# Performance work log

Hardware: AMD Instinct MI355X
Metric: run time of the kernel (lower is better)

## Reference

```python
import jax, jax.numpy as jnp
import numpy as np

N, E, G = 100000, 1600000, 8
IN, H, OUT = 3, 64, 20


def setup_inputs() -> dict:
    key = jax.random.key(0)
    ks = jax.random.split(key, 24)
    def nrm(k, shape, scale=0.1):
        return jax.random.normal(k, shape, dtype=jnp.float32) * scale
    inp = {}
    inp["x"] = jax.random.normal(ks[0], (N, IN), dtype=jnp.float32)
    inp["edge_index"] = jax.random.randint(ks[1], (2, E), 0, N, dtype=jnp.int32)
    inp["batch"] = jnp.sort(jax.random.randint(ks[2], (N,), 0, G, dtype=jnp.int32))
    dims = [(IN, H), (H, H), (H, H)]  # 3 GATConv layers (initial + layers-1)
    for i, (di, do) in enumerate(dims):
        inp[f"W{i}"] = nrm(ks[3 + 4 * i], (di, do))
        inp[f"as{i}"] = nrm(ks[4 + 4 * i], (do,))
        inp[f"ad{i}"] = nrm(ks[5 + 4 * i], (do,))
        inp[f"b{i}"] = jnp.zeros((do,), jnp.float32)
    inp["vn_emb0"] = jnp.zeros((1, H), jnp.float32)  # constant-0 init per module
    inp["m1_w1"] = nrm(ks[15], (H, H)); inp["m1_b1"] = jnp.zeros((H,), jnp.float32)
    inp["m1_w2"] = nrm(ks[16], (H, H)); inp["m1_b2"] = jnp.zeros((H,), jnp.float32)
    inp["mf_w1"] = nrm(ks[17], (H, H)); inp["mf_b1"] = jnp.zeros((H,), jnp.float32)
    inp["mf_w2"] = nrm(ks[18], (H, OUT)); inp["mf_b2"] = jnp.zeros((OUT,), jnp.float32)
    inp["out_w"] = nrm(ks[19], (H, OUT)); inp["out_b"] = jnp.zeros((OUT,), jnp.float32)
    return inp


def _gat(x, src, dst, W, a_s, a_d, b):
    # PyG GATConv, 1 head: h = xW; e_ij = LeakyReLU_0.2(a_s.h_j + a_d.h_i);
    # alpha = softmax over incoming edges of each dst node; out_i = sum_j alpha_ij h_j + b
    h = x @ W                                                  # [N, H]
    lg = jax.nn.leaky_relu((h @ a_s)[src] + (h @ a_d)[dst], 0.2)  # [E+N]
    m = jax.ops.segment_max(lg, dst, num_segments=N)
    m = jnp.where(jnp.isfinite(m), m, 0.0)
    p = jnp.exp(lg - m[dst])
    denom = jax.ops.segment_sum(p, dst, num_segments=N)
    alpha = p / denom[dst]
    return jax.ops.segment_sum(alpha[:, None] * h[src], dst, num_segments=N) + b


def _forward(x, edge_index, batch, params):
    (W0, as0, ad0, b0, W1, as1, ad1, b1, W2, as2, ad2, b2,
     vn_emb0, m1_w1, m1_b1, m1_w2, m1_b2, mf_w1, mf_b1, mf_w2, mf_b2,
     out_w, out_b) = params
    loops = jnp.arange(N, dtype=edge_index.dtype)  # GATConv add_self_loops=True
    src = jnp.concatenate([edge_index[0], loops])
    dst = jnp.concatenate([edge_index[1], loops])
    act = lambda v: jax.nn.leaky_relu(v, 0.01)  # nn.LeakyReLU default slope
    h = act(_gat(x, src, dst, W0, as0, ad0, b0))
    h = act(_gat(h, src, dst, W1, as1, ad1, b1))
    h = act(_gat(h, src, dst, W2, as2, ad2, b2))
    # virtual node: global_add_pool(out, batch) + Embedding(0) (zero-init)
    vn = jax.ops.segment_sum(h, batch, num_segments=G) + vn_emb0[0]
    vn = jax.nn.relu(vn @ m1_w1 + m1_b1)
    vn = jax.nn.relu(vn @ m1_w2 + m1_b2)
    vn = jax.nn.relu(vn @ mf_w1 + mf_b1)
    vn = jax.nn.relu(vn @ mf_w2 + mf_b2)
    return (h @ out_w + out_b, vn)


def reference(x, edge_index, batch, W0, as0, ad0, b0, W1, as1, ad1, b1,
              W2, as2, ad2, b2, vn_emb0, m1_w1, m1_b1, m1_w2, m1_b2,
              mf_w1, mf_b1, mf_w2, mf_b2, out_w, out_b):
    params = (W0, as0, ad0, b0, W1, as1, ad1, b1, W2, as2, ad2, b2,
              vn_emb0, m1_w1, m1_b1, m1_w2, m1_b2, mf_w1, mf_b1, mf_w2, mf_b2,
              out_w, out_b)
    return _forward(x, edge_index, batch, params)
```

## Files before the change

kernel.cpp:

```cpp
#include <hip/hip_runtime.h>
#include <hip/hip_bf16.h>

#define H 64
#define OUTD 20
#define NGRAPH 8
#define NBK 256
#define CAPB 8192
#define MAXDEG 63

typedef __attribute__((ext_vector_type(8))) short bf16x8;
typedef __attribute__((ext_vector_type(4))) float f32x4;
typedef __attribute__((ext_vector_type(8))) unsigned short u16x8;


__device__ __forceinline__ float ldp(const void* p, int i, bool f32) {
    return f32 ? ((const float*)p)[i]
               : __bfloat162float(((const __hip_bfloat16*)p)[i]);
}

__device__ __forceinline__ float bfu(unsigned short u) {
    union { unsigned int i; float f; } c; c.i = ((unsigned)u) << 16; return c.f;
}
__device__ __forceinline__ unsigned short fbits(float f) {
    __hip_bfloat16 b = __float2bfloat16(f);
    return *reinterpret_cast<unsigned short*>(&b);
}

__global__ void detect_dtype(const unsigned short* __restrict__ xb, int n_u16,
                             int* __restrict__ flag, int* __restrict__ gcur,
                             int* __restrict__ gtot, float* __restrict__ vnp,
                             float* __restrict__ s, short* __restrict__ hbuf,
                             int n, int ns) {
    __shared__ int sh[256];
    int t = threadIdx.x;
    int m = min(n_u16, 4096);
    int bad = 0;
    for (int i = t; i < m; i += 256) {
        unsigned e = (xb[i] >> 7) & 0xFF;
        bad += (e >= 0x90) ? 1 : 0;
    }
    sh[t] = bad;
    if (t < NBK) gcur[t] = 0;
    for (int i = t; i < NGRAPH * H; i += 256) vnp[i] = 0.f;
    if (t < 32) hbuf[(size_t)n * 32 + t] = 0;
    else if (t < 64) hbuf[((size_t)ns + n) * 32 + (t - 32)] = 0;
    if (t == 0) { *gtot = 0; s[n] = -1e30f; }
    __syncthreads();
    for (int off = 128; off; off >>= 1) {
        if (t < off) sh[t] += sh[t + off];
        __syncthreads();
    }
    if (t == 0) *flag = (sh[0] > (m >> 4)) ? 1 : 0;
}

__global__ void fillC_dense0(const int* __restrict__ src, const int* __restrict__ dst,
                             int* __restrict__ gcur, unsigned* __restrict__ ebuf,
                             int E, int n, int ns, int nC, int EPC, int nbk,
                             const void* __restrict__ x, const void* __restrict__ W,
                             const void* __restrict__ a_s, const void* __restrict__ a_d,
                             __hip_bfloat16* __restrict__ h, float* __restrict__ s,
                             float* __restrict__ d, const int* __restrict__ flagp) {
    if ((int)blockIdx.x < nC) {
        __shared__ unsigned lcnt[NBK];
        __shared__ int lbase[NBK];
        int t = threadIdx.x;
        for (int i = t; i < NBK; i += 256) lcnt[i] = 0;
        __syncthreads();
        int base = blockIdx.x * (256 * EPC) + t;
        int dnr[8];
        for (int i = 0; i < EPC; ++i) {
            int e = base + i * 256;
            int dn = (e < E) ? dst[e] : -1;
            if (i < 8) dnr[i] = dn;
            if ((unsigned)dn < (unsigned)n) atomicAdd(&lcnt[dn >> 9], 1u);
        }
        __syncthreads();
        for (int i = t; i < nbk; i += 256) {
            unsigned c = lcnt[i];
            lbase[i] = c ? atomicAdd(&gcur[i], (int)c) : 0;
            lcnt[i] = 0;
        }
        __syncthreads();
        for (int i = 0; i < EPC; ++i) {
            int e = base + i * 256;
            if (e < E) {
                int dn = (i < 8) ? dnr[i] : dst[e];
                if ((unsigned)dn < (unsigned)n) {
                    int b = dn >> 9;
                    unsigned pos = (unsigned)lbase[b] + atomicAdd(&lcnt[b], 1u);
                    if (pos < CAPB)
                        ebuf[(size_t)b * CAPB + pos] =
                            ((unsigned)src[e] << 9) | (unsigned)(dn & 511);
                }
            }
        }
        return;
    }
    const bool f32 = (*flagp != 0);
    int idx = ((int)blockIdx.x - nC) * 256 + threadIdx.x;
    int node = idx >> 6;
    int f = idx & 63;
    if (node >= n) return;
    float acc = 0.f;
    for (int k = 0; k < 3; ++k)
        acc += ldp(x, node * 3 + k, f32) * ldp(W, k * H + f, f32);
    ((short*)h)[((size_t)(f >> 5) * ns + node) * 32 + (f & 31)] = (short)fbits(acc);
    float sv = acc * ldp(a_s, f, f32);
    float dv = acc * ldp(a_d, f, f32);
    for (int off = 32; off; off >>= 1) {
        sv += __shfl_xor(sv, off);
        dv += __shfl_xor(dv, off);
    }
    if (f == 0) { s[node] = sv; d[node] = dv; }
}

__global__ __launch_bounds__(512) void bucketD(const unsigned* __restrict__ ebuf,
                                               const int* __restrict__ gcur,
                                               unsigned* __restrict__ cntoff,
                                               int* __restrict__ col,
                                               int* __restrict__ gtot, int n) {
    __shared__ unsigned lcnt[512];
    __shared__ int loff[512];
    __shared__ int sdeg[512];
    __shared__ int wpart[8];
    __shared__ int sbase, stot;
    int b = blockIdx.x, t = threadIdx.x;
    lcnt[t] = 0;
    __syncthreads();
    int end = min(gcur[b], CAPB);
    const unsigned* reg = ebuf + (size_t)b * CAPB;
    for (int i = t; i < end; i += 512) atomicAdd(&lcnt[reg[i] & 511u], 1u);
    __syncthreads();
    int node = (b << 9) + t;
    int degc = (node < n) ? (int)min(lcnt[t], (unsigned)MAXDEG) : 0;
    int Dp = (node < n) ? ((degc + 1 <= 24) ? 24 : 64) : 0;
    int lane = t & 63, wid = t >> 6;
    int xs = Dp;
    for (int o = 1; o < 64; o <<= 1) {
        int v = __shfl_up(xs, o);
        if (lane >= o) xs += v;
    }
    if (lane == 63) wpart[wid] = xs;
    __syncthreads();
    if (t == 0) {
        int acc = 0;
        for (int w8 = 0; w8 < 8; ++w8) { int v = wpart[w8]; wpart[w8] = acc; acc += v; }
        stot = acc;
        sbase = atomicAdd(gtot, acc);
    }
    __syncthreads();
    int myoff = sbase + wpart[wid] + xs - Dp;
    loff[t] = myoff;
    sdeg[t] = degc;
    if (node < n) cntoff[node] = (unsigned)myoff | ((unsigned)Dp << 24);
    lcnt[t] = 0;
    int total = stot;
    for (int i = t; i < total; i += 512) col[sbase + i] = n;
    __syncthreads();
    if (node < n) col[myoff + degc] = node;
    for (int i = t; i < end; i += 512) {
        unsigned e = reg[i];
        int loc = (int)(e & 511u);
        unsigned pos = atomicAdd(&lcnt[loc], 1u);
        if ((int)pos < sdeg[loc])
            col[loff[loc] + pos] = (int)(e >> 9);
    }
}

#define ACC8(w, hv) { \
    a[0] += w * bfu(hv[0]); a[1] += w * bfu(hv[1]); \
    a[2] += w * bfu(hv[2]); a[3] += w * bfu(hv[3]); \
    a[4] += w * bfu(hv[4]); a[5] += w * bfu(hv[5]); \
    a[6] += w * bfu(hv[6]); a[7] += w * bfu(hv[7]); }

__global__ void gat_agg_sliced(const short* __restrict__ hs,
                               const float* __restrict__ s,
                               const float* __restrict__ d,
                               const unsigned* __restrict__ cntoff,
                               const int* __restrict__ col,
                               const void* __restrict__ bias,
                               short* __restrict__ outs, int n, int ns,
                               const int* __restrict__ flagp) {
    const bool f32 = (*flagp != 0);
    int shp = (int)blockIdx.x & 7;
    int fh = shp >> 2, nq = shp & 3;
    int qN = (n + 3) >> 2;
    int node = nq * qN + ((int)blockIdx.x >> 3) * 8 + ((int)threadIdx.x >> 5);
    int lim = min(n, (nq + 1) * qN);
    if (node >= lim) return;
    int l = threadIdx.x & 31;
    int c = l & 3, q = l >> 2;
    unsigned co = cntoff[node];
    bool big = (int)(co >> 24) > 24;
    const int* cb = col + (co & 0xFFFFFFu);
    const char* hb = (const char*)hs + (size_t)fh * ns * 64;
    float di = d[node];
    unsigned coff = (unsigned)c * 16u;

    int s0 = cb[q];
    int s1 = cb[q + 8];
    int s2 = cb[q + 16];
    float v0 = s[s0] + di, v1 = s[s1] + di, v2 = s[s2] + di;
    u16x8 hv0 = *(const u16x8*)(hb + ((unsigned)s0 * 64u + coff));
    u16x8 hv1 = *(const u16x8*)(hb + ((unsigned)s1 * 64u + coff));
    u16x8 hv2 = *(const u16x8*)(hb + ((unsigned)s2 * 64u + coff));
    float sv0 = v0 > 0.f ? v0 : 0.2f * v0;
    float sv1 = v1 > 0.f ? v1 : 0.2f * v1;
    float sv2 = v2 > 0.f ? v2 : 0.2f * v2;

    float sv3 = -INFINITY, sv4 = -INFINITY, sv5 = -INFINITY,
          sv6 = -INFINITY, sv7 = -INFINITY;
    u16x8 hv3 = {}, hv4 = {}, hv5 = {}, hv6 = {}, hv7 = {};
    if (big) {
        int s3 = cb[q + 24];
        int s4 = cb[q + 32];
        int s5 = cb[q + 40];
        int s6 = cb[q + 48];
        int s7 = cb[q + 56];
        float v3 = s[s3] + di, v4 = s[s4] + di, v5 = s[s5] + di,
              v6 = s[s6] + di, v7 = s[s7] + di;
        hv3 = *(const u16x8*)(hb + ((unsigned)s3 * 64u + coff));
        hv4 = *(const u16x8*)(hb + ((unsigned)s4 * 64u + coff));
        hv5 = *(const u16x8*)(hb + ((unsigned)s5 * 64u + coff));
        hv6 = *(const u16x8*)(hb + ((unsigned)s6 * 64u + coff));
        hv7 = *(const u16x8*)(hb + ((unsigned)s7 * 64u + coff));
        sv3 = v3 > 0.f ? v3 : 0.2f * v3;
        sv4 = v4 > 0.f ? v4 : 0.2f * v4;
        sv5 = v5 > 0.f ? v5 : 0.2f * v5;
        sv6 = v6 > 0.f ? v6 : 0.2f * v6;
        sv7 = v7 > 0.f ? v7 : 0.2f * v7;
    }

    float mx = fmaxf(fmaxf(fmaxf(sv0, sv1), fmaxf(sv2, sv3)),
                     fmaxf(fmaxf(sv4, sv5), fmaxf(sv6, sv7)));
    mx = fmaxf(mx, __shfl_xor(mx, 4));
    mx = fmaxf(mx, __shfl_xor(mx, 8));
    mx = fmaxf(mx, __shfl_xor(mx, 16));

    float w0 = __expf(sv0 - mx);
    float w1 = __expf(sv1 - mx);
    float w2 = __expf(sv2 - mx);
    float wsum = w0 + w1 + w2;

    float a[8] = {0.f, 0.f, 0.f, 0.f, 0.f, 0.f, 0.f, 0.f};
    ACC8(w0, hv0);
    ACC8(w1, hv1);
    ACC8(w2, hv2);
    if (big) {
        float w3 = __expf(sv3 - mx);
        float w4 = __expf(sv4 - mx);
        float w5 = __expf(sv5 - mx);
        float w6 = __expf(sv6 - mx);
        float w7 = __expf(sv7 - mx);
        wsum += w3 + w4 + w5 + w6 + w7;
        ACC8(w3, hv3);
        ACC8(w4, hv4);
        ACC8(w5, hv5);
        ACC8(w6, hv6);
        ACC8(w7, hv7);
    }
    wsum += __shfl_xor(wsum, 4);
    wsum += __shfl_xor(wsum, 8);
    wsum += __shfl_xor(wsum, 16);
#pragma unroll
    for (int i = 0; i < 8; ++i) {
        a[i] += __shfl_xor(a[i], 4);
        a[i] += __shfl_xor(a[i], 8);
        a[i] += __shfl_xor(a[i], 16);
    }
    if (q == 0) {
        float inv = 1.f / fmaxf(wsum, 1e-20f);
        u16x8 ov;
        for (int i = 0; i < 8; ++i) {
            float o = a[i] * inv + ldp(bias, fh * 32 + c * 8 + i, f32);
            o = o > 0.f ? o : 0.01f * o;
            ov[i] = fbits(o);
        }
        ((u16x8*)outs)[((size_t)fh * ns + node) * 4 + c] = ov;
    }
}


__global__ __launch_bounds__(256) void denseN_mfma(
    const __hip_bfloat16* __restrict__ in,
    const void* __restrict__ W,
    const void* __restrict__ a_s, const void* __restrict__ a_d,
    __hip_bfloat16* __restrict__ h, float* __restrict__ s,
    float* __restrict__ d, int n, int ns, const int* __restrict__ flagp) {
    const bool f32 = (*flagp != 0);
    __shared__ short Wt[64 * 72];
    int t = threadIdx.x;
    for (int i = t; i < 4096; i += 256) {
        int k = i >> 6, nf = i & 63;
        Wt[nf * 72 + k] = (short)fbits(ldp(W, i, f32));
    }
    __syncthreads();

    int wid = t >> 6, lane = t & 63;
    int quad = lane >> 4, n16 = lane & 15;
    int nodeBase = blockIdx.x * 64 + wid * 16;
    int mrow = nodeBase + n16;
    int mclamp = min(mrow, n - 1);
    const short* inp = (const short*)in;
    bf16x8 a0 = *(const bf16x8*)(inp + (size_t)mclamp * 32 + quad * 8);
    bf16x8 a1 = *(const bf16x8*)(inp + ((size_t)ns + mclamp) * 32 + quad * 8);

    float as_v[4], ad_v[4];
    for (int nt = 0; nt < 4; ++nt) {
        as_v[nt] = ldp(a_s, nt * 16 + n16, f32);
        ad_v[nt] = ldp(a_d, nt * 16 + n16, f32);
    }

    float sv[4] = {0.f, 0.f, 0.f, 0.f}, dv[4] = {0.f, 0.f, 0.f, 0.f};
    f32x4 accs[4];
    for (int nt = 0; nt < 4; ++nt) {
        const short* wrow = Wt + (nt * 16 + n16) * 72;
        bf16x8 b0 = *(const bf16x8*)(wrow + quad * 8);
        bf16x8 b1 = *(const bf16x8*)(wrow + 32 + quad * 8);
        f32x4 cacc = {0.f, 0.f, 0.f, 0.f};
        cacc = __builtin_amdgcn_mfma_f32_16x16x32_bf16(a0, b0, cacc, 0, 0, 0);
        cacc = __builtin_amdgcn_mfma_f32_16x16x32_bf16(a1, b1, cacc, 0, 0, 0);
        accs[nt] = cacc;
        for (int r = 0; r < 4; ++r) {
            sv[r] += cacc[r] * as_v[nt];
            dv[r] += cacc[r] * ad_v[nt];
        }
    }

    short* hb = (short*)h;
    for (int r = 0; r < 4; ++r) {
        int node = nodeBase + quad * 4 + r;
        if (node < n) {
            for (int nt = 0; nt < 4; ++nt) {
                int f = nt * 16 + n16;
                hb[((size_t)(f >> 5) * ns + node) * 32 + (f & 31)] = (short)fbits(accs[nt][r]);
            }
        }
    }
    for (int r = 0; r < 4; ++r) {
        for (int mask = 1; mask < 16; mask <<= 1) {
            sv[r] += __shfl_xor(sv[r], mask);
            dv[r] += __shfl_xor(dv[r], mask);
        }
    }
    if (n16 == 0) {
        for (int r = 0; r < 4; ++r) {
            int node = nodeBase + quad * 4 + r;
            if (node < n) { s[node] = sv[r]; d[node] = dv[r]; }
        }
    }
}


__global__ __launch_bounds__(256) void proj_pool(
    const __hip_bfloat16* __restrict__ h,
    const void* __restrict__ W, const void* __restrict__ b,
    void* __restrict__ out, int n, int ns, const int* __restrict__ flagp,
    int projBlocks, const int* __restrict__ batch, float* __restrict__ vn) {
    const bool f32 = (*flagp != 0);
    if ((int)blockIdx.x < projBlocks) {
        __shared__ short Wt[32 * 72];
        int t = threadIdx.x;
        for (int i = t; i < 32 * 64; i += 256) {
            int o = i >> 6, k = i & 63;
            Wt[o * 72 + k] = (o < OUTD) ? (short)fbits(ldp(W, k * OUTD + o, f32)) : 0;
        }
        __syncthreads();

        int wid = t >> 6, lane = t & 63;
        int quad = lane >> 4, n16 = lane & 15;
        int nodeBase = blockIdx.x * 64 + wid * 16;
        int mclamp = min(nodeBase + n16, n - 1);
        const short* hsrc = (const short*)h;
        bf16x8 a0 = *(const bf16x8*)(hsrc + (size_t)mclamp * 32 + quad * 8);
        bf16x8 a1 = *(const bf16x8*)(hsrc + ((size_t)ns + mclamp) * 32 + quad * 8);

        f32x4 acc0 = {0.f, 0.f, 0.f, 0.f}, acc1 = {0.f, 0.f, 0.f, 0.f};
        {
            const short* wrow = Wt + n16 * 72;
            bf16x8 b0 = *(const bf16x8*)(wrow + quad * 8);
            bf16x8 b1 = *(const bf16x8*)(wrow + 32 + quad * 8);
            acc0 = __builtin_amdgcn_mfma_f32_16x16x32_bf16(a0, b0, acc0, 0, 0, 0);
            acc0 = __builtin_amdgcn_mfma_f32_16x16x32_bf16(a1, b1, acc0, 0, 0, 0);
        }
        {
            const short* wrow = Wt + (16 + n16) * 72;
            bf16x8 b0 = *(const bf16x8*)(wrow + quad * 8);
            bf16x8 b1 = *(const bf16x8*)(wrow + 32 + quad * 8);
            acc1 = __builtin_amdgcn_mfma_f32_16x16x32_bf16(a0, b0, acc1, 0, 0, 0);
            acc1 = __builtin_amdgcn_mfma_f32_16x16x32_bf16(a1, b1, acc1, 0, 0, 0);
        }
        float bv0 = ldp(b, n16, f32);
        float bv1 = (n16 < OUTD - 16) ? ldp(b, 16 + n16, f32) : 0.f;
        for (int r = 0; r < 4; ++r) {
            int node = nodeBase + quad * 4 + r;
            if (node >= n) break;
            float o0 = acc0[r] + bv0;
            if (f32) ((float*)out)[node * OUTD + n16] = o0;
            else     ((__hip_bfloat16*)out)[node * OUTD + n16] = __float2bfloat16(o0);
            if (n16 < OUTD - 16) {
                float o1 = acc1[r] + bv1;
                if (f32) ((float*)out)[node * OUTD + 16 + n16] = o1;
                else     ((__hip_bfloat16*)out)[node * OUTD + 16 + n16] = __float2bfloat16(o1);
            }
        }
        return;
    }
    __shared__ float part[NGRAPH * H];
    int t = threadIdx.x;
    for (int i = t; i < NGRAPH * H; i += 256) part[i] = 0.f;
    __syncthreads();
    int pb = (int)blockIdx.x - projBlocks;
    int npb = gridDim.x - projBlocks;
    int wid = t >> 6, lane = t & 63;
    int gwave = pb * 4 + wid;
    int nwaves = npb * 4;
    int chunk = (n + nwaves - 1) / nwaves;
    int beg = gwave * chunk;
    int end = min(n, beg + chunk);
    if (beg < end) {
        const short* hb = (const short*)h + (size_t)(lane >> 5) * ns * 32 + (lane & 31);
        float acc = 0.f;
        int cur = batch[beg];
        for (int i = beg; i < end; ++i) {
            int g = batch[i];
            if (g != cur) {
                if ((unsigned)cur < NGRAPH) atomicAdd(&part[cur * H + lane], acc);
                acc = 0.f;
                cur = g;
            }
            acc += bfu((unsigned short)hb[(size_t)i * 32]);
        }
        if ((unsigned)cur < NGRAPH) atomicAdd(&part[cur * H + lane], acc);
    }
    __syncthreads();
    for (int i = t; i < NGRAPH * H; i += 256) {
        float v = part[i];
        if (v != 0.f) atomicAdd(&vn[i], v);
    }
}


__global__ void vn_mlp(const float* __restrict__ vn, const void* __restrict__ emb,
                       const void* __restrict__ w1, const void* __restrict__ b1,
                       const void* __restrict__ w2, const void* __restrict__ b2,
                       const void* __restrict__ w3, const void* __restrict__ b3,
                       const void* __restrict__ w4, const void* __restrict__ b4,
                       void* __restrict__ out, int out1_off, const int* __restrict__ flagp) {
    const bool f32 = (*flagp != 0);
    __shared__ float A[NGRAPH * H], B[NGRAPH * H];
    int t = threadIdx.x;
    int g = t >> 6, f = t & 63;
    A[t] = vn[t] + ldp(emb, f, f32);
    __syncthreads();
    float acc = ldp(b1, f, f32);
    for (int k = 0; k < H; ++k) acc += A[g * H + k] * ldp(w1, k * H + f, f32);
    B[t] = fmaxf(acc, 0.f);
    __syncthreads();
    acc = ldp(b2, f, f32);
    for (int k = 0; k < H; ++k) acc += B[g * H + k] * ldp(w2, k * H + f, f32);
    A[t] = fmaxf(acc, 0.f);
    __syncthreads();
    acc = ldp(b3, f, f32);
    for (int k = 0; k < H; ++k) acc += A[g * H + k] * ldp(w3, k * H + f, f32);
    B[t] = fmaxf(acc, 0.f);
    __syncthreads();
    if (f < OUTD) {
        acc = ldp(b4, f, f32);
        for (int k = 0; k < H; ++k) acc += B[g * H + k] * ldp(w4, k * OUTD + f, f32);
        acc = fmaxf(acc, 0.f);
        int idx = out1_off + g * OUTD + f;
        if (f32) ((float*)out)[idx] = acc;
        else     ((__hip_bfloat16*)out)[idx] = __float2bfloat16(acc);
    }
}


extern "C" void kernel_launch(void* const* d_in, const int* in_sizes, int n_in,
                              void* d_out, int out_size, void* d_ws, size_t ws_size,
                              hipStream_t stream) {
    const void* x   = d_in[0];
    const int* ei   = (const int*)d_in[1];
    const int* batch= (const int*)d_in[2];
    const void* W0  = d_in[3];
    const void* as0 = d_in[4];
    const void* ad0 = d_in[5];
    const void* b0  = d_in[6];
    const void* W1  = d_in[7];
    const void* as1 = d_in[8];
    const void* ad1 = d_in[9];
    const void* b1  = d_in[10];
    const void* W2  = d_in[11];
    const void* as2 = d_in[12];
    const void* ad2 = d_in[13];
    const void* b2  = d_in[14];
    const void* vne = d_in[15];
    const void* m1w1 = d_in[16];
    const void* m1b1 = d_in[17];
    const void* m1w2 = d_in[18];
    const void* m1b2 = d_in[19];
    const void* mfw1 = d_in[20];
    const void* mfb1 = d_in[21];
    const void* mfw2 = d_in[22];
    const void* mfb2 = d_in[23];
    const void* outw = d_in[24];
    const void* outb = d_in[25];

    const int N = in_sizes[2];
    const int E = in_sizes[1] / 2;
    const int NS = N + 1;
    const int* srcp = ei;
    const int* dstp = ei + E;

    char* w = (char*)d_ws;
    auto alloc = [&](size_t bytes) -> void* {
        void* p = (void*)w;
        w += ((bytes + 255) / 256) * 256;
        return p;
    };
    int*   flag   = (int*)alloc(256);
    int*   gcur   = (int*)alloc((size_t)NBK * 4);
    int*   gtot   = (int*)alloc(256);
    unsigned* ebuf= (unsigned*)alloc((size_t)NBK * CAPB * 4);
    unsigned* cntoff = (unsigned*)alloc((size_t)N * 4);
    int*   col    = (int*)alloc(((size_t)N * 64 + 64) * 4);
    __hip_bfloat16* featA = (__hip_bfloat16*)alloc((size_t)NS * H * 2);
    __hip_bfloat16* featB = (__hip_bfloat16*)alloc((size_t)NS * H * 2);
    __hip_bfloat16* hbuf  = (__hip_bfloat16*)alloc((size_t)NS * H * 2);
    float* sArr   = (float*)alloc((size_t)NS * 4);
    float* dArr   = (float*)alloc((size_t)N * 4);
    float* vn     = (float*)alloc((size_t)NGRAPH * H * 4);

    const int nbN64 = (N * H + 255) / 256;
    const int nb64 = (N + 63) / 64;
    const int projBlocks = (N + 63) / 64;
    const int nbk = (N + 511) >> 9;
    const int qN = (N + 3) >> 2;
    const int aggBlocks = 8 * ((qN + 7) / 8);
    int EPC = 8;
    int nC = (E + 256 * EPC - 1) / (256 * EPC);
    while (nC > 1024) { EPC <<= 1; nC = (E + 256 * EPC - 1) / (256 * EPC); }

    detect_dtype<<<1, 256, 0, stream>>>((const unsigned short*)x, in_sizes[0], flag,
                                        gcur, gtot, vn, sArr, (short*)hbuf, N, NS);

    fillC_dense0<<<nC + nbN64, 256, 0, stream>>>(
        srcp, dstp, gcur, ebuf, E, N, NS, nC, EPC, nbk,
        x, W0, as0, ad0, hbuf, sArr, dArr, flag);
    bucketD<<<nbk, 512, 0, stream>>>(ebuf, gcur, cntoff, col, gtot, N);

    gat_agg_sliced<<<aggBlocks, 256, 0, stream>>>((const short*)hbuf, sArr, dArr,
                                                  cntoff, col, b0, (short*)featA, N, NS, flag);
    denseN_mfma<<<nb64, 256, 0, stream>>>(featA, W1, as1, ad1, hbuf, sArr, dArr, N, NS, flag);
    gat_agg_sliced<<<aggBlocks, 256, 0, stream>>>((const short*)hbuf, sArr, dArr,
                                                  cntoff, col, b1, (short*)featB, N, NS, flag);
    denseN_mfma<<<nb64, 256, 0, stream>>>(featB, W2, as2, ad2, hbuf, sArr, dArr, N, NS, flag);
    gat_agg_sliced<<<aggBlocks, 256, 0, stream>>>((const short*)hbuf, sArr, dArr,
                                                  cntoff, col, b2, (short*)featA, N, NS, flag);

    proj_pool<<<projBlocks + 512, 256, 0, stream>>>(featA, outw, outb, d_out, N, NS, flag,
                                                    projBlocks, batch, vn);
    vn_mlp<<<1, 512, 0, stream>>>(vn, vne, m1w1, m1b1, m1w2, m1b2, mfw1, mfb1, mfw2, mfb2,
                                  d_out, N * OUTD, flag);
}
```

Measured before the change: 427.2 us.

## Split features into four 16-wide slices and aggregate with two lanes per node

Changes the bf16 feature layout from two 32-feature slices to four 16-feature slices (32 bytes per node row) across all producer and consumer kernels. The aggregation kernel now assigns two lanes per node per quarter slice, each lane walking the node's neighbour list serially. Degree-24 nodes take an unrolled path; other nodes use an online-softmax loop over blocks of 8. This drops the cross-lane shuffle reductions and makes each gather smaller, but adds serial per-lane work and more total index and score loads, since every slice re-reads the neighbour list.

```diff
diff --git a/kernel.cpp b/kernel.cpp
--- a/kernel.cpp
+++ b/kernel.cpp
@@ -42,8 +42,8 @@
     sh[t] = bad;
     if (t < NBK) gcur[t] = 0;
     for (int i = t; i < NGRAPH * H; i += 256) vnp[i] = 0.f;
-    if (t < 32) hbuf[(size_t)n * 32 + t] = 0;
-    else if (t < 64) hbuf[((size_t)ns + n) * 32 + (t - 32)] = 0;
+    if (t < 64)
+        hbuf[(size_t)(t >> 4) * ns * 16 + (size_t)n * 16 + (t & 15)] = 0;
     if (t == 0) { *gtot = 0; s[n] = -1e30f; }
     __syncthreads();
     for (int off = 128; off; off >>= 1) {
@@ -104,7 +104,8 @@
     float acc = 0.f;
     for (int k = 0; k < 3; ++k)
         acc += ldp(x, node * 3 + k, f32) * ldp(W, k * H + f, f32);
-    ((short*)h)[((size_t)(f >> 5) * ns + node) * 32 + (f & 31)] = (short)fbits(acc);
+    ((short*)h)[(size_t)(f >> 4) * ns * 16 + (size_t)node * 16 + (f & 15)] =
+        (short)fbits(acc);
     float sv = acc * ldp(a_s, f, f32);
     float dv = acc * ldp(a_d, f, f32);
     for (int off = 32; off; off >>= 1) {
@@ -167,117 +168,122 @@
     }
 }
 
-#define ACC8(w, hv) { \
-    a[0] += w * bfu(hv[0]); a[1] += w * bfu(hv[1]); \
-    a[2] += w * bfu(hv[2]); a[3] += w * bfu(hv[3]); \
-    a[4] += w * bfu(hv[4]); a[5] += w * bfu(hv[5]); \
-    a[6] += w * bfu(hv[6]); a[7] += w * bfu(hv[7]); }
-
-__global__ void gat_agg_sliced(const short* __restrict__ hs,
-                               const float* __restrict__ s,
-                               const float* __restrict__ d,
-                               const unsigned* __restrict__ cntoff,
-                               const int* __restrict__ col,
-                               const void* __restrict__ bias,
-                               short* __restrict__ outs, int n, int ns,
-                               const int* __restrict__ flagp) {
+__global__ void gat_agg_q(const short* __restrict__ hs,
+                          const float* __restrict__ s,
+                          const float* __restrict__ d,
+                          const unsigned* __restrict__ cntoff,
+                          const int* __restrict__ col,
+                          const void* __restrict__ bias,
+                          short* __restrict__ outs, int n, int ns, int halfN,
+                          const int* __restrict__ flagp) {
     const bool f32 = (*flagp != 0);
     int shp = (int)blockIdx.x & 7;
-    int fh = shp >> 2, nq = shp & 3;
-    int qN = (n + 3) >> 2;
-    int node = nq * qN + ((int)blockIdx.x >> 3) * 8 + ((int)threadIdx.x >> 5);
-    int lim = min(n, (nq + 1) * qN);
+    int fq = shp >> 1, nh = shp & 1;
+    int node = nh * halfN + ((int)blockIdx.x >> 3) * 128 + ((int)threadIdx.x >> 1);
+    int lim = nh ? n : halfN;
     if (node >= lim) return;
-    int l = threadIdx.x & 31;
-    int c = l & 3, q = l >> 2;
+    int c = threadIdx.x & 1;
     unsigned co = cntoff[node];
-    bool big = (int)(co >> 24) > 24;
     const int* cb = col + (co & 0xFFFFFFu);
-    const char* hb = (const char*)hs + (size_t)fh * ns * 64;
+    const char* hq = (const char*)hs + (size_t)fq * ns * 32 + c * 16;
     float di = d[node];
-    unsigned coff = (unsigned)c * 16u;
-
-    int s0 = cb[q];
-    int s1 = cb[q + 8];
-    int s2 = cb[q + 16];
-    float v0 = s[s0] + di, v1 = s[s1] + di, v2 = s[s2] + di;
-    u16x8 hv0 = *(const u16x8*)(hb + ((unsigned)s0 * 64u + coff));
-    u16x8 hv1 = *(const u16x8*)(hb + ((unsigned)s1 * 64u + coff));
-    u16x8 hv2 = *(const u16x8*)(hb + ((unsigned)s2 * 64u + coff));
-    float sv0 = v0 > 0.f ? v0 : 0.2f * v0;
-    float sv1 = v1 > 0.f ? v1 : 0.2f * v1;
-    float sv2 = v2 > 0.f ? v2 : 0.2f * v2;
-
-    float sv3 = -INFINITY, sv4 = -INFINITY, sv5 = -INFINITY,
-          sv6 = -INFINITY, sv7 = -INFINITY;
-    u16x8 hv3 = {}, hv4 = {}, hv5 = {}, hv6 = {}, hv7 = {};
-    if (big) {
-        int s3 = cb[q + 24];
-        int s4 = cb[q + 32];
-        int s5 = cb[q + 40];
-        int s6 = cb[q + 48];
-        int s7 = cb[q + 56];
-        float v3 = s[s3] + di, v4 = s[s4] + di, v5 = s[s5] + di,
-              v6 = s[s6] + di, v7 = s[s7] + di;
-        hv3 = *(const u16x8*)(hb + ((unsigned)s3 * 64u + coff));
-        hv4 = *(const u16x8*)(hb + ((unsigned)s4 * 64u + coff));
-        hv5 = *(const u16x8*)(hb + ((unsigned)s5 * 64u + coff));
-        hv6 = *(const u16x8*)(hb + ((unsigned)s6 * 64u + coff));
-        hv7 = *(const u16x8*)(hb + ((unsigned)s7 * 64u + coff));
-        sv3 = v3 > 0.f ? v3 : 0.2f * v3;
-        sv4 = v4 > 0.f ? v4 : 0.2f * v4;
-        sv5 = v5 > 0.f ? v5 : 0.2f * v5;
-        sv6 = v6 > 0.f ? v6 : 0.2f * v6;
-        sv7 = v7 > 0.f ? v7 : 0.2f * v7;
-    }
-
-    float mx = fmaxf(fmaxf(fmaxf(sv0, sv1), fmaxf(sv2, sv3)),
-                     fmaxf(fmaxf(sv4, sv5), fmaxf(sv6, sv7)));
-    mx = fmaxf(mx, __shfl_xor(mx, 4));
-    mx = fmaxf(mx, __shfl_xor(mx, 8));
-    mx = fmaxf(mx, __shfl_xor(mx, 16));
-
-    float w0 = __expf(sv0 - mx);
-    float w1 = __expf(sv1 - mx);
-    float w2 = __expf(sv2 - mx);
-    float wsum = w0 + w1 + w2;
-
-    float a[8] = {0.f, 0.f, 0.f, 0.f, 0.f, 0.f, 0.f, 0.f};
-    ACC8(w0, hv0);
-    ACC8(w1, hv1);
-    ACC8(w2, hv2);
-    if (big) {
-        float w3 = __expf(sv3 - mx);
-        float w4 = __expf(sv4 - mx);
-        float w5 = __expf(sv5 - mx);
-        float w6 = __expf(sv6 - mx);
-        float w7 = __expf(sv7 - mx);
-        wsum += w3 + w4 + w5 + w6 + w7;
-        ACC8(w3, hv3);
-        ACC8(w4, hv4);
-        ACC8(w5, hv5);
-        ACC8(w6, hv6);
-        ACC8(w7, hv7);
-    }
-    wsum += __shfl_xor(wsum, 4);
-    wsum += __shfl_xor(wsum, 8);
-    wsum += __shfl_xor(wsum, 16);
-#pragma unroll
-    for (int i = 0; i < 8; ++i) {
-        a[i] += __shfl_xor(a[i], 4);
-        a[i] += __shfl_xor(a[i], 8);
-        a[i] += __shfl_xor(a[i], 16);
-    }
-    if (q == 0) {
-        float inv = 1.f / fmaxf(wsum, 1e-20f);
-        u16x8 ov;
-        for (int i = 0; i < 8; ++i) {
-            float o = a[i] * inv + ldp(bias, fh * 32 + c * 8 + i, f32);
-            o = o > 0.f ? o : 0.01f * o;
-            ov[i] = fbits(o);
-        }
-        ((u16x8*)outs)[((size_t)fh * ns + node) * 4 + c] = ov;
-    }
+
+    float acc0 = 0.f, acc1 = 0.f, acc2 = 0.f, acc3 = 0.f,
+          acc4 = 0.f, acc5 = 0.f, acc6 = 0.f, acc7 = 0.f;
+    float wsum = 0.f;
+
+#define FMA8(w, hv) { \
+    acc0 += w * bfu(hv[0]); acc1 += w * bfu(hv[1]); \
+    acc2 += w * bfu(hv[2]); acc3 += w * bfu(hv[3]); \
+    acc4 += w * bfu(hv[4]); acc5 += w * bfu(hv[5]); \
+    acc6 += w * bfu(hv[6]); acc7 += w * bfu(hv[7]); }
+
+    if ((co >> 24) == 24u) {
+        int sc[24];
+#pragma unroll
+        for (int k = 0; k < 24; ++k) sc[k] = __builtin_nontemporal_load(cb + k);
+        float sv[24];
+#pragma unroll
+        for (int k = 0; k < 24; ++k) {
+            float v = s[sc[k]] + di;
+            sv[k] = v > 0.f ? v : 0.2f * v;
+        }
+        float m12[12];
+#pragma unroll
+        for (int k = 0; k < 12; ++k) m12[k] = fmaxf(sv[2 * k], sv[2 * k + 1]);
+        float m6[6];
+#pragma unroll
+        for (int k = 0; k < 6; ++k) m6[k] = fmaxf(m12[2 * k], m12[2 * k + 1]);
+        float mx = fmaxf(fmaxf(fmaxf(m6[0], m6[1]), fmaxf(m6[2], m6[3])),
+                         fmaxf(m6[4], m6[5]));
+#pragma unroll
+        for (int b = 0; b < 3; ++b) {
+            u16x8 hv[8];
+#pragma unroll
+            for (int k = 0; k < 8; ++k)
+                hv[k] = *(const u16x8*)(hq + (unsigned)sc[b * 8 + k] * 32u);
+#pragma unroll
+            for (int k = 0; k < 8; ++k) {
+                float w = __expf(sv[b * 8 + k] - mx);
+                wsum += w;
+                FMA8(w, hv[k]);
+            }
+        }
+    } else {
+        float mx = -1e28f;
+#pragma unroll 1
+        for (int b = 0; b < 8; ++b) {
+            int sc[8];
+#pragma unroll
+            for (int k = 0; k < 8; ++k)
+                sc[k] = __builtin_nontemporal_load(cb + b * 8 + k);
+            float sv[8];
+#pragma unroll
+            for (int k = 0; k < 8; ++k) {
+                float v = s[sc[k]] + di;
+                sv[k] = v > 0.f ? v : 0.2f * v;
+            }
+            u16x8 hv[8];
+#pragma unroll
+            for (int k = 0; k < 8; ++k)
+                hv[k] = *(const u16x8*)(hq + (unsigned)sc[k] * 32u);
+            float bmx = fmaxf(fmaxf(fmaxf(sv[0], sv[1]), fmaxf(sv[2], sv[3])),
+                              fmaxf(fmaxf(sv[4], sv[5]), fmaxf(sv[6], sv[7])));
+            float mxn = fmaxf(mx, bmx);
+            float scale = __expf(mx - mxn);
+            wsum *= scale;
+            acc0 *= scale; acc1 *= scale; acc2 *= scale; acc3 *= scale;
+            acc4 *= scale; acc5 *= scale; acc6 *= scale; acc7 *= scale;
+#pragma unroll
+            for (int k = 0; k < 8; ++k) {
+                float w = __expf(sv[k] - mxn);
+                wsum += w;
+                FMA8(w, hv[k]);
+            }
+            mx = mxn;
+        }
+    }
+
+    float inv = 1.f / fmaxf(wsum, 1e-20f);
+    u16x8 ov;
+    float o0 = acc0 * inv + ldp(bias, fq * 16 + c * 8 + 0, f32);
+    float o1 = acc1 * inv + ldp(bias, fq * 16 + c * 8 + 1, f32);
+    float o2 = acc2 * inv + ldp(bias, fq * 16 + c * 8 + 2, f32);
+    float o3 = acc3 * inv + ldp(bias, fq * 16 + c * 8 + 3, f32);
+    float o4 = acc4 * inv + ldp(bias, fq * 16 + c * 8 + 4, f32);
+    float o5 = acc5 * inv + ldp(bias, fq * 16 + c * 8 + 5, f32);
+    float o6 = acc6 * inv + ldp(bias, fq * 16 + c * 8 + 6, f32);
+    float o7 = acc7 * inv + ldp(bias, fq * 16 + c * 8 + 7, f32);
+    ov[0] = fbits(o0 > 0.f ? o0 : 0.01f * o0);
+    ov[1] = fbits(o1 > 0.f ? o1 : 0.01f * o1);
+    ov[2] = fbits(o2 > 0.f ? o2 : 0.01f * o2);
+    ov[3] = fbits(o3 > 0.f ? o3 : 0.01f * o3);
+    ov[4] = fbits(o4 > 0.f ? o4 : 0.01f * o4);
+    ov[5] = fbits(o5 > 0.f ? o5 : 0.01f * o5);
+    ov[6] = fbits(o6 > 0.f ? o6 : 0.01f * o6);
+    ov[7] = fbits(o7 > 0.f ? o7 : 0.01f * o7);
+    ((u16x8*)outs)[((size_t)fq * ns + node) * 2 + c] = ov;
+#undef FMA8
 }
 
 
@@ -302,8 +308,10 @@
     int mrow = nodeBase + n16;
     int mclamp = min(mrow, n - 1);
     const short* inp = (const short*)in;
-    bf16x8 a0 = *(const bf16x8*)(inp + (size_t)mclamp * 32 + quad * 8);
-    bf16x8 a1 = *(const bf16x8*)(inp + ((size_t)ns + mclamp) * 32 + quad * 8);
+    bf16x8 a0 = *(const bf16x8*)(inp + (size_t)(quad >> 1) * ns * 16 +
+                                 (size_t)mclamp * 16 + (quad & 1) * 8);
+    bf16x8 a1 = *(const bf16x8*)(inp + (size_t)(2 + (quad >> 1)) * ns * 16 +
+                                 (size_t)mclamp * 16 + (quad & 1) * 8);
 
     float as_v[4], ad_v[4];
     for (int nt = 0; nt < 4; ++nt) {
@@ -333,7 +341,8 @@
         if (node < n) {
             for (int nt = 0; nt < 4; ++nt) {
                 int f = nt * 16 + n16;
-                hb[((size_t)(f >> 5) * ns + node) * 32 + (f & 31)] = (short)fbits(accs[nt][r]);
+                hb[(size_t)(f >> 4) * ns * 16 + (size_t)node * 16 + (f & 15)] =
+                    (short)fbits(accs[nt][r]);
             }
         }
     }
@@ -372,8 +381,10 @@
         int nodeBase = blockIdx.x * 64 + wid * 16;
         int mclamp = min(nodeBase + n16, n - 1);
         const short* hsrc = (const short*)h;
-        bf16x8 a0 = *(const bf16x8*)(hsrc + (size_t)mclamp * 32 + quad * 8);
-        bf16x8 a1 = *(const bf16x8*)(hsrc + ((size_t)ns + mclamp) * 32 + quad * 8);
+        bf16x8 a0 = *(const bf16x8*)(hsrc + (size_t)(quad >> 1) * ns * 16 +
+                                     (size_t)mclamp * 16 + (quad & 1) * 8);
+        bf16x8 a1 = *(const bf16x8*)(hsrc + (size_t)(2 + (quad >> 1)) * ns * 16 +
+                                     (size_t)mclamp * 16 + (quad & 1) * 8);
 
         f32x4 acc0 = {0.f, 0.f, 0.f, 0.f}, acc1 = {0.f, 0.f, 0.f, 0.f};
         {
@@ -419,7 +430,7 @@
     int beg = gwave * chunk;
     int end = min(n, beg + chunk);
     if (beg < end) {
-        const short* hb = (const short*)h + (size_t)(lane >> 5) * ns * 32 + (lane & 31);
+        const short* hb = (const short*)h + (size_t)(lane >> 4) * ns * 16 + (lane & 15);
         float acc = 0.f;
         int cur = batch[beg];
         for (int i = beg; i < end; ++i) {
@@ -429,7 +440,7 @@
                 acc = 0.f;
                 cur = g;
             }
-            acc += bfu((unsigned short)hb[(size_t)i * 32]);
+            acc += bfu((unsigned short)hb[(size_t)i * 16]);
         }
         if ((unsigned)cur < NGRAPH) atomicAdd(&part[cur * H + lane], acc);
     }
@@ -535,8 +546,8 @@
     const int nb64 = (N + 63) / 64;
     const int projBlocks = (N + 63) / 64;
     const int nbk = (N + 511) >> 9;
-    const int qN = (N + 3) >> 2;
-    const int aggBlocks = 8 * ((qN + 7) / 8);
+    const int halfN = (N + 1) / 2;
+    const int aggBlocks = 8 * ((halfN + 127) / 128);
     int EPC = 8;
     int nC = (E + 256 * EPC - 1) / (256 * EPC);
     while (nC > 1024) { EPC <<= 1; nC = (E + 256 * EPC - 1) / (256 * EPC); }
@@ -549,14 +560,17 @@
         x, W0, as0, ad0, hbuf, sArr, dArr, flag);
     bucketD<<<nbk, 512, 0, stream>>>(ebuf, gcur, cntoff, col, gtot, N);
 
-    gat_agg_sliced<<<aggBlocks, 256, 0, stream>>>((const short*)hbuf, sArr, dArr,
-                                                  cntoff, col, b0, (short*)featA, N, NS, flag);
+    gat_agg_q<<<aggBlocks, 256, 0, stream>>>((const short*)hbuf, sArr, dArr,
+                                             cntoff, col, b0, (short*)featA,
+                                             N, NS, halfN, flag);
     denseN_mfma<<<nb64, 256, 0, stream>>>(featA, W1, as1, ad1, hbuf, sArr, dArr, N, NS, flag);
-    gat_agg_sliced<<<aggBlocks, 256, 0, stream>>>((const short*)hbuf, sArr, dArr,
-                                                  cntoff, col, b1, (short*)featB, N, NS, flag);
+    gat_agg_q<<<aggBlocks, 256, 0, stream>>>((const short*)hbuf, sArr, dArr,
+                                             cntoff, col, b1, (short*)featB,
+                                             N, NS, halfN, flag);
     denseN_mfma<<<nb64, 256, 0, stream>>>(featB, W2, as2, ad2, hbuf, sArr, dArr, N, NS, flag);
-    gat_agg_sliced<<<aggBlocks, 256, 0, stream>>>((const short*)hbuf, sArr, dArr,
-                                                  cntoff, col, b2, (short*)featA, N, NS, flag);
+    gat_agg_q<<<aggBlocks, 256, 0, stream>>>((const short*)hbuf, sArr, dArr,
+                                             cntoff, col, b2, (short*)featA,
+                                             N, NS, halfN, flag);
 
     proj_pool<<<projBlocks + 512, 256, 0, stream>>>(featA, outw, outb, d_out, N, NS, flag,
                                                     projBlocks, batch, vn);
```

Measured after the change: 560.2 us. 31.2% more time.
